# Kernel optimization log

Hardware: AMD Instinct MI355X
Metric: run time of the kernel (lower is better)

Reference implementation:

```python
import jax, jax.numpy as jnp
import numpy as np

NH, NKV, D = 16, 8, 128
HID = 2048
EPS = 1e-6
ROPE_BASE = 10000.0
T = 2048


def setup_inputs() -> dict:
    key = jax.random.key(0)
    k1, k2, k3 = jax.random.split(key, 3)
    return {
        "positions": jnp.arange(T, dtype=jnp.int32),
        "hidden_states": jax.random.normal(k1, (T, HID), dtype=jnp.float32),
        "w_qkv": jax.random.normal(k2, (HID, (NH + 2 * NKV) * D), dtype=jnp.float32) * 0.02,
        "w_o": jax.random.normal(k3, (NH * D, HID), dtype=jnp.float32) * 0.02,
        "q_norm_w": jnp.ones((D,), dtype=jnp.float32),
        "k_norm_w": jnp.ones((D,), dtype=jnp.float32),
    }


def _rmsnorm(x, w):
    # per-head RMSNorm over last dim (head_dim)
    return x * jax.lax.rsqrt(jnp.mean(x * x, axis=-1, keepdims=True) + EPS) * w


def reference(positions, hidden_states, w_qkv, w_o, q_norm_w, k_norm_w):
    t = hidden_states.shape[0]
    scale = D ** -0.5

    # fused QKV projection, then split
    qkv = hidden_states @ w_qkv                       # [T, (NH+2*NKV)*D]
    q, k, v = jnp.split(qkv, [NH * D, (NH + NKV) * D], axis=-1)
    q = q.reshape(t, NH, D)
    k = k.reshape(t, NKV, D)
    v = v.reshape(t, NKV, D)

    # per-head QK RMSNorm (Qwen3)
    q = _rmsnorm(q, q_norm_w)
    k = _rmsnorm(k, k_norm_w)

    # RoPE (neox style: rotate half-split pairs)
    inv_freq = 1.0 / (ROPE_BASE ** (jnp.arange(0, D, 2, dtype=jnp.float32) / D))
    freqs = positions.astype(jnp.float32)[:, None] * inv_freq  # [T, D/2]
    cos = jnp.cos(freqs)[:, None, :]                   # [T, 1, D/2]
    sin = jnp.sin(freqs)[:, None, :]

    def rope(x):
        x1, x2 = jnp.split(x, 2, axis=-1)
        return jnp.concatenate([x1 * cos - x2 * sin, x2 * cos + x1 * sin], axis=-1)

    q = rope(q)
    k = rope(k)

    # GQA: repeat kv heads
    g = NH // NKV
    kr = jnp.repeat(k, g, axis=1)                      # [T, NH, D]
    vr = jnp.repeat(v, g, axis=1)

    # causal attention
    scores = jnp.einsum('thd,shd->hts', q, kr) * scale  # [NH, T, T]
    causal = jnp.tril(jnp.ones((t, t), dtype=bool))
    scores = jnp.where(causal[None], scores, -jnp.inf)
    probs = jax.nn.softmax(scores, axis=-1)
    o = jnp.einsum('hts,shd->thd', probs, vr).reshape(t, NH * D)

    return o @ w_o
```

## Files before the change

kernel.cpp:

```cpp
#include <hip/hip_runtime.h>
#include <math.h>

#define T_TOK 2048
#define HIDDEN 2048
#define NH 16
#define NKV 8
#define DH 128

typedef unsigned short u16;
typedef __attribute__((ext_vector_type(8))) short bf16x8;
typedef __attribute__((ext_vector_type(4))) float f32x4;

__device__ __forceinline__ u16 f2bf(float f) {
  union { float f; unsigned u; } x; x.f = f;
  unsigned r = (x.u + 0x7fffu + ((x.u >> 16) & 1u)) >> 16;
  return (u16)r;
}

__device__ __forceinline__ void gload16(const void* g, void* l) {
  __builtin_amdgcn_global_load_lds((const __attribute__((address_space(1))) void*)g,
                                   (__attribute__((address_space(3))) void*)l,
                                   16, 0, 0);
}

__global__ __launch_bounds__(256) void prepass(const float* __restrict__ hidden,
                                               const float* __restrict__ w_qkv,
                                               const float* __restrict__ w_o,
                                               u16* __restrict__ Xb,
                                               u16* __restrict__ WqkvT,
                                               u16* __restrict__ WoT) {
  __shared__ float tile[64][65];
  const int b = blockIdx.x;
  if (b < 4096) {
    int i = b * 256 + threadIdx.x;
    float4 v = ((const float4*)hidden)[i];
    ushort4 o;
    o.x = f2bf(v.x); o.y = f2bf(v.y); o.z = f2bf(v.z); o.w = f2bf(v.w);
    ((ushort4*)Xb)[i] = o;
    return;
  }
  const float* in; u16* out; int R, Cdim, c0, r0;
  if (b < 6144) {
    int bb = b - 4096;
    in = w_qkv; out = WqkvT; R = 2048; Cdim = 4096;
    c0 = (bb & 63) * 64; r0 = (bb >> 6) * 64;
  } else {
    int bb = b - 6144;
    in = w_o; out = WoT; R = 2048; Cdim = 2048;
    c0 = (bb & 31) * 64; r0 = (bb >> 5) * 64;
  }
  const int tx = threadIdx.x & 63, ty = threadIdx.x >> 6;
#pragma unroll
  for (int i = 0; i < 64; i += 4)
    tile[ty + i][tx] = in[(size_t)(r0 + ty + i) * Cdim + c0 + tx];
  __syncthreads();
#pragma unroll
  for (int i = 0; i < 64; i += 4)
    out[(size_t)(c0 + ty + i) * R + r0 + tx] = f2bf(tile[tx][ty + i]);
}

__global__ __launch_bounds__(256) void add_f32_vec(const float* __restrict__ a,
                                                   const float* __restrict__ b,
                                                   float* __restrict__ o, int n4) {
  int i = blockIdx.x * blockDim.x + threadIdx.x;
  if (i < n4) {
    float4 x = ((const float4*)a)[i], y = ((const float4*)b)[i];
    float4 z = {x.x + y.x, x.y + y.y, x.z + y.z, x.w + y.w};
    ((float4*)o)[i] = z;
  }
}

__global__ __launch_bounds__(256) void rope_vt(const float* __restrict__ qkv,
                                               const int* __restrict__ pos,
                                               const float* __restrict__ qw,
                                               const float* __restrict__ kw,
                                               u16* __restrict__ Qg,
                                               u16* __restrict__ Kg,
                                               u16* __restrict__ Vt,
                                               unsigned* __restrict__ counter) {
  __shared__ float tile[64][65];
  const int b = blockIdx.x;
  if (b < 12288) {
    const int wave = threadIdx.x >> 6, j = threadIdx.x & 63;
    const int idx = b * 4 + wave;
    const int t = idx & 2047, slot = idx >> 11;
    const float QSC = 0.088388347648318447f * 1.4426950408889634f;
    const float* src = qkv + (size_t)t * 4096 + slot * 128;
    float x1 = src[j], x2 = src[j + 64];
    float ss = x1 * x1 + x2 * x2;
#pragma unroll
    for (int m = 1; m < 64; m <<= 1) ss += __shfl_xor(ss, m);
    float r = rsqrtf(ss * (1.0f / 128.0f) + 1e-6f);
    const bool isq = slot < NH;
    const float* w = isq ? qw : kw;
    float xn1 = x1 * r * w[j], xn2 = x2 * r * w[j + 64];
    float fp = (float)pos[t];
    float inv_freq = exp2f(-(float)j * (13.287712379549449f / 64.0f));
    float ang = fp * inv_freq;
    float sn, cs;
    sincosf(ang, &sn, &cs);
    float o1 = xn1 * cs - xn2 * sn;
    float o2 = xn2 * cs + xn1 * sn;
    if (isq) {
      size_t base = ((size_t)slot * T_TOK + t) * DH;
      Qg[base + j] = f2bf(o1 * QSC); Qg[base + 64 + j] = f2bf(o2 * QSC);
    } else {
      size_t base = ((size_t)(slot - NH) * T_TOK + t) * DH;
      Kg[base + j] = f2bf(o1); Kg[base + 64 + j] = f2bf(o2);
    }
    return;
  }
  if (b == 12288 && threadIdx.x == 0) *counter = 0u;
  const int bb = b - 12288;
  const int h = bb & 7, rest = bb >> 3;
  const int t0 = (rest & 31) * 64, d0 = (rest >> 5) * 64;
  const int tx = threadIdx.x & 63, ty = threadIdx.x >> 6;
#pragma unroll
  for (int i = 0; i < 64; i += 4)
    tile[ty + i][tx] = qkv[(size_t)(t0 + ty + i) * 4096 + (NH + NKV) * DH + h * DH + d0 + tx];
  __syncthreads();
#pragma unroll
  for (int i = 0; i < 64; i += 4)
    Vt[((size_t)h * DH + d0 + ty + i) * T_TOK + t0 + tx] = f2bf(tile[tx][ty + i]);
}

__global__ __launch_bounds__(256) void gemm_bf16(const u16* __restrict__ A,
                                                 const u16* __restrict__ Bt,
                                                 float* __restrict__ C,
                                                 int M, int N, int K, int lda, int ldb) {
  __shared__ u16 Alds[128 * 32];
  __shared__ u16 Blds[128 * 32];
  A += (size_t)blockIdx.z * K;
  Bt += (size_t)blockIdx.z * K;
  C += (size_t)blockIdx.z * M * N;
  const int m0 = blockIdx.y * 128, n0 = blockIdx.x * 128;
  const int wave = threadIdx.x >> 6, lane = threadIdx.x & 63;
  const int l15 = lane & 15, quad = lane >> 4;
  const int wr = wave >> 1, wc = wave & 1;

  const f32x4 zero = {0.f, 0.f, 0.f, 0.f};
  f32x4 acc[4][4];
#pragma unroll
  for (int i = 0; i < 4; ++i)
#pragma unroll
    for (int j = 0; j < 4; ++j) acc[i][j] = zero;

  for (int k0 = 0; k0 < K; k0 += 32) {
    __syncthreads();
#pragma unroll
    for (int c = 0; c < 2; ++c) {
      int chunk = wave * 2 + c;
      int slot = chunk * 64 + lane;
      int row = slot >> 2;
      int g = (slot & 3) ^ (row & 3);
      gload16(A + (size_t)(m0 + row) * lda + k0 + g * 8, &Alds[chunk * 512]);
      gload16(Bt + (size_t)(n0 + row) * ldb + k0 + g * 8, &Blds[chunk * 512]);
    }
    __syncthreads();
    bf16x8 af[4], bfr[4];
#pragma unroll
    for (int mt = 0; mt < 4; ++mt) {
      int r = wr * 64 + mt * 16 + l15;
      af[mt] = *(const bf16x8*)&Alds[r * 32 + ((quad ^ (r & 3)) * 8)];
    }
#pragma unroll
    for (int nt = 0; nt < 4; ++nt) {
      int r = wc * 64 + nt * 16 + l15;
      bfr[nt] = *(const bf16x8*)&Blds[r * 32 + ((quad ^ (r & 3)) * 8)];
    }
#pragma unroll
    for (int mt = 0; mt < 4; ++mt)
#pragma unroll
      for (int nt = 0; nt < 4; ++nt)
        acc[mt][nt] = __builtin_amdgcn_mfma_f32_16x16x32_bf16(af[mt], bfr[nt], acc[mt][nt], 0, 0, 0);
  }
#pragma unroll
  for (int mt = 0; mt < 4; ++mt)
#pragma unroll
    for (int nt = 0; nt < 4; ++nt)
#pragma unroll
      for (int r = 0; r < 4; ++r)
        C[(size_t)(m0 + wr * 64 + mt * 16 + quad * 4 + r) * N + n0 + wc * 64 + nt * 16 + l15] =
            acc[mt][nt][r];
}

__global__ __launch_bounds__(256) void attn_kernel(const u16* __restrict__ Qg,
                                                   const u16* __restrict__ Kg,
                                                   const u16* __restrict__ Vtg,
                                                   float* __restrict__ Opart,
                                                   float* __restrict__ Lpart,
                                                   unsigned* __restrict__ counter) {
  __shared__ u16 Klds[64 * 128];
  __shared__ u16 Vlds[128 * 64];
  __shared__ u16 Plds[4][16 * 72];
  __shared__ unsigned item_s;
  const int wave = threadIdx.x >> 6, lane = threadIdx.x & 63;
  const int l15 = lane & 15, quad = lane >> 4;
  u16* Pw = &Plds[wave][0];
  const f32x4 zero = {0.f, 0.f, 0.f, 0.f};
  const float4 zero4 = {0.f, 0.f, 0.f, 0.f};

  for (;;) {
    __syncthreads();
    if (threadIdx.x == 0) item_s = atomicAdd(counter, 1u);
    __syncthreads();
    const unsigned item = item_s;
    if (item >= 1024u) break;
    const int qt = 31 - (int)(item >> 5);
    const int s  = (int)(item >> 4) & 1;
    const int h  = (int)item & 15;
    const int kvh = h >> 1;
    const int slot = (h * 32 + qt) * 2 + s;
    const int j0 = s ? (qt + 2) >> 1 : 0;
    const int j1 = s ? qt + 1 : (qt + 2) >> 1;

    float* Oslot = Opart + (size_t)slot * (64 * 128);

    if (j0 >= j1) {
      for (int t = threadIdx.x; t < 64 * 128 / 4; t += 256) ((float4*)Oslot)[t] = zero4;
      if (threadIdx.x < 64) Lpart[slot * 64 + threadIdx.x] = 0.f;
      continue;
    }

    const u16* Qh = Qg + (size_t)h * T_TOK * DH;
    const u16* Kh = Kg + (size_t)kvh * T_TOK * DH;
    const u16* Vh = Vtg + (size_t)kvh * DH * T_TOK;
    const int qrow0 = qt * 64 + wave * 16;

    bf16x8 qf[4];
#pragma unroll
    for (int ks = 0; ks < 4; ++ks)
      qf[ks] = *(const bf16x8*)(Qh + (size_t)(qrow0 + l15) * DH + ks * 32 + quad * 8);

    f32x4 oacc[8];
#pragma unroll
    for (int i = 0; i < 8; ++i) oacc[i] = zero;
    float l_i[4] = {0.f, 0.f, 0.f, 0.f};

    for (int j = j0; j < j1; ++j) {
      __syncthreads();
#pragma unroll
      for (int c = 0; c < 4; ++c) {
        int chunk = wave * 4 + c;
        int sl = chunk * 64 + lane;
        {
          int ss = sl >> 4;
          int g = (sl & 15) ^ (ss & 15);
          gload16(Kh + ((size_t)(j * 64 + ss)) * DH + g * 8, &Klds[chunk * 512]);
        }
        {
          int d = sl >> 3;
          int g = (sl & 7) ^ (d & 7);
          gload16(Vh + (size_t)d * T_TOK + j * 64 + g * 8, &Vlds[chunk * 512]);
        }
      }
      __syncthreads();

      f32x4 sacc[4];
#pragma unroll
      for (int nt = 0; nt < 4; ++nt) sacc[nt] = zero;
#pragma unroll
      for (int nt = 0; nt < 4; ++nt) {
        int sr = nt * 16 + l15;
#pragma unroll
        for (int ks = 0; ks < 4; ++ks) {
          bf16x8 kf = *(const bf16x8*)&Klds[sr * 128 + (((ks * 4 + quad) ^ (sr & 15)) * 8)];
          sacc[nt] = __builtin_amdgcn_mfma_f32_16x16x32_bf16(qf[ks], kf, sacc[nt], 0, 0, 0);
        }
      }

      if (j == qt) {
#pragma unroll
        for (int nt = 0; nt < 4; ++nt)
#pragma unroll
          for (int r = 0; r < 4; ++r) {
            int col = j * 64 + nt * 16 + l15;
            int row = qrow0 + quad * 4 + r;
            if (col > row) sacc[nt][r] = -INFINITY;
          }
      }

#pragma unroll
      for (int nt = 0; nt < 4; ++nt)
#pragma unroll
        for (int r = 0; r < 4; ++r) {
          float pv = exp2f(sacc[nt][r]);
          unsigned u = __float_as_uint(pv);
          Pw[(quad * 4 + r) * 72 + nt * 16 + l15] = (u16)(u >> 16);
          l_i[r] += __uint_as_float(u & 0xffff0000u);
        }

      bf16x8 pf[2];
#pragma unroll
      for (int ks = 0; ks < 2; ++ks)
        pf[ks] = *(const bf16x8*)&Pw[l15 * 72 + ks * 32 + quad * 8];
#pragma unroll
      for (int ot = 0; ot < 8; ++ot) {
        int d = ot * 16 + l15;
#pragma unroll
        for (int ks = 0; ks < 2; ++ks) {
          bf16x8 vf = *(const bf16x8*)&Vlds[d * 64 + (((ks * 4 + quad) ^ (d & 7)) * 8)];
          oacc[ot] = __builtin_amdgcn_mfma_f32_16x16x32_bf16(pf[ks], vf, oacc[ot], 0, 0, 0);
        }
      }
    }

#pragma unroll
    for (int ot = 0; ot < 8; ++ot)
#pragma unroll
      for (int r = 0; r < 4; ++r)
        Oslot[(wave * 16 + quad * 4 + r) * 128 + ot * 16 + l15] = oacc[ot][r];
#pragma unroll
    for (int msk = 1; msk < 16; msk <<= 1)
#pragma unroll
      for (int r = 0; r < 4; ++r) l_i[r] += __shfl_xor(l_i[r], msk);
    if (l15 == 0) {
#pragma unroll
      for (int r = 0; r < 4; ++r)
        Lpart[slot * 64 + wave * 16 + quad * 4 + r] = l_i[r];
    }
  }
}

__global__ __launch_bounds__(256) void attn_merge(const float* __restrict__ Opart,
                                                  const float* __restrict__ Lpart,
                                                  u16* __restrict__ Og) {
  const int b = blockIdx.x;
  const int h = b & 15, qt = b >> 4;
  const int slot0 = (h * 32 + qt) * 2, slot1 = slot0 + 1;
  const float4* O0 = (const float4*)(Opart + (size_t)slot0 * (64 * 128));
  const float4* O1 = (const float4*)(Opart + (size_t)slot1 * (64 * 128));
#pragma unroll
  for (int it = 0; it < 8; ++it) {
    int idx = it * 256 + threadIdx.x;
    int r = idx >> 5, c4 = idx & 31;
    float rl = 1.0f / (Lpart[slot0 * 64 + r] + Lpart[slot1 * 64 + r]);
    float4 a = O0[idx], c = O1[idx];
    int row = qt * 64 + r, col = c4 * 4;
    u16* dst = Og + (size_t)row * (NH * DH) + h * DH + col;
    dst[0] = f2bf((a.x + c.x) * rl);
    dst[1] = f2bf((a.y + c.y) * rl);
    dst[2] = f2bf((a.z + c.z) * rl);
    dst[3] = f2bf((a.w + c.w) * rl);
  }
}

extern "C" void kernel_launch(void* const* d_in, const int* in_sizes, int n_in,
                              void* d_out, int out_size, void* d_ws, size_t ws_size,
                              hipStream_t stream) {
  (void)in_sizes; (void)n_in; (void)out_size; (void)ws_size;
  const int* positions = (const int*)d_in[0];
  const float* hidden  = (const float*)d_in[1];
  const float* w_qkv   = (const float*)d_in[2];
  const float* w_o     = (const float*)d_in[3];
  const float* q_norm  = (const float*)d_in[4];
  const float* k_norm  = (const float*)d_in[5];
  float* out = (float*)d_out;

  char* ws = (char*)d_ws;
  u16*   Xb    = (u16*)(ws);
  u16*   WqkvT = (u16*)(ws + ( 8ull << 20));
  u16*   WoT   = (u16*)(ws + (24ull << 20));
  float* QKV   = (float*)(ws + (32ull << 20));
  u16*   Qg    = (u16*)(ws + (64ull << 20));
  u16*   Kg    = (u16*)(ws + (72ull << 20));
  u16*   Vt    = (u16*)(ws + (76ull << 20));
  u16*   AttnO = (u16*)(ws + (80ull << 20));
  float* Opart = QKV;
  float* Lpart = (float*)(ws);
  unsigned* ctr = (unsigned*)(ws + (512ull << 10));
  float* G2P0  = QKV;
  float* G2P1  = QKV + 2048 * 2048;

  prepass<<<dim3(7168), 256, 0, stream>>>(hidden, w_qkv, w_o, Xb, WqkvT, WoT);

  gemm_bf16<<<dim3(4096 / 128, T_TOK / 128, 1), 256, 0, stream>>>(
      Xb, WqkvT, QKV, T_TOK, 4096, HIDDEN, HIDDEN, HIDDEN);

  rope_vt<<<dim3(12288 + 512), 256, 0, stream>>>(QKV, positions, q_norm, k_norm, Qg, Kg, Vt, ctr);

  attn_kernel<<<dim3(768), 256, 0, stream>>>(Qg, Kg, Vt, Opart, Lpart, ctr);
  attn_merge<<<dim3(512), 256, 0, stream>>>(Opart, Lpart, AttnO);

  gemm_bf16<<<dim3(HIDDEN / 128, T_TOK / 128, 2), 256, 0, stream>>>(
      AttnO, WoT, G2P0, T_TOK, HIDDEN, 1024, NH * DH, NH * DH);
  add_f32_vec<<<dim3(T_TOK * HIDDEN / 4 / 256), 256, 0, stream>>>(
      G2P0, G2P1, out, T_TOK * HIDDEN / 4);
}
```

Before: 272.2 us.

## Deepen GEMM K-tile to 64 and add split-K for QKV and output GEMMs

The bf16 GEMM now stages 64-wide K slices in LDS with an 8-way XOR swizzle and runs two MFMA sub-steps per barrier pair, which halves the number of synchronisations per K. When the workspace is large enough, the QKV projection is split along K into two partial outputs that rope_vt sums on load, and the output projection uses a 4-way split-K reduced by a generalized add kernel. These splits are meant to raise the number of blocks in flight, at the cost of extra fp32 partial traffic and larger LDS use per block.

```diff
diff --git a/kernel.cpp b/kernel.cpp
--- a/kernel.cpp
+++ b/kernel.cpp
@@ -59,18 +59,26 @@
     out[(size_t)(c0 + ty + i) * R + r0 + tx] = f2bf(tile[tx][ty + i]);
 }
 
-__global__ __launch_bounds__(256) void add_f32_vec(const float* __restrict__ a,
-                                                   const float* __restrict__ b,
-                                                   float* __restrict__ o, int n4) {
+__global__ __launch_bounds__(256) void add_parts(const float* __restrict__ a,
+                                                 const float* __restrict__ b,
+                                                 const float* __restrict__ c,
+                                                 const float* __restrict__ d,
+                                                 float* __restrict__ o, int n4, int nparts) {
   int i = blockIdx.x * blockDim.x + threadIdx.x;
   if (i < n4) {
     float4 x = ((const float4*)a)[i], y = ((const float4*)b)[i];
     float4 z = {x.x + y.x, x.y + y.y, x.z + y.z, x.w + y.w};
+    if (nparts == 4) {
+      float4 u = ((const float4*)c)[i], v = ((const float4*)d)[i];
+      z.x += u.x + v.x; z.y += u.y + v.y; z.z += u.z + v.z; z.w += u.w + v.w;
+    }
     ((float4*)o)[i] = z;
   }
 }
 
-__global__ __launch_bounds__(256) void rope_vt(const float* __restrict__ qkv,
+__global__ __launch_bounds__(256) void rope_vt(const float* __restrict__ qkv0,
+                                               const float* __restrict__ qkv1,
+                                               int sumP,
                                                const int* __restrict__ pos,
                                                const float* __restrict__ qw,
                                                const float* __restrict__ kw,
@@ -85,8 +93,9 @@
     const int idx = b * 4 + wave;
     const int t = idx & 2047, slot = idx >> 11;
     const float QSC = 0.088388347648318447f * 1.4426950408889634f;
-    const float* src = qkv + (size_t)t * 4096 + slot * 128;
-    float x1 = src[j], x2 = src[j + 64];
+    const size_t base_i = (size_t)t * 4096 + slot * 128;
+    float x1 = qkv0[base_i + j], x2 = qkv0[base_i + j + 64];
+    if (sumP) { x1 += qkv1[base_i + j]; x2 += qkv1[base_i + j + 64]; }
     float ss = x1 * x1 + x2 * x2;
 #pragma unroll
     for (int m = 1; m < 64; m <<= 1) ss += __shfl_xor(ss, m);
@@ -116,8 +125,12 @@
   const int t0 = (rest & 31) * 64, d0 = (rest >> 5) * 64;
   const int tx = threadIdx.x & 63, ty = threadIdx.x >> 6;
 #pragma unroll
-  for (int i = 0; i < 64; i += 4)
-    tile[ty + i][tx] = qkv[(size_t)(t0 + ty + i) * 4096 + (NH + NKV) * DH + h * DH + d0 + tx];
+  for (int i = 0; i < 64; i += 4) {
+    size_t gi = (size_t)(t0 + ty + i) * 4096 + (NH + NKV) * DH + h * DH + d0 + tx;
+    float v = qkv0[gi];
+    if (sumP) v += qkv1[gi];
+    tile[ty + i][tx] = v;
+  }
   __syncthreads();
 #pragma unroll
   for (int i = 0; i < 64; i += 4)
@@ -128,8 +141,8 @@
                                                  const u16* __restrict__ Bt,
                                                  float* __restrict__ C,
                                                  int M, int N, int K, int lda, int ldb) {
-  __shared__ u16 Alds[128 * 32];
-  __shared__ u16 Blds[128 * 32];
+  __shared__ u16 Alds[128 * 64];
+  __shared__ u16 Blds[128 * 64];
   A += (size_t)blockIdx.z * K;
   Bt += (size_t)blockIdx.z * K;
   C += (size_t)blockIdx.z * M * N;
@@ -145,34 +158,37 @@
 #pragma unroll
     for (int j = 0; j < 4; ++j) acc[i][j] = zero;
 
-  for (int k0 = 0; k0 < K; k0 += 32) {
+  for (int k0 = 0; k0 < K; k0 += 64) {
     __syncthreads();
 #pragma unroll
-    for (int c = 0; c < 2; ++c) {
-      int chunk = wave * 2 + c;
+    for (int c = 0; c < 4; ++c) {
+      int chunk = wave * 4 + c;
       int slot = chunk * 64 + lane;
-      int row = slot >> 2;
-      int g = (slot & 3) ^ (row & 3);
+      int row = slot >> 3;
+      int g = (slot & 7) ^ (row & 7);
       gload16(A + (size_t)(m0 + row) * lda + k0 + g * 8, &Alds[chunk * 512]);
       gload16(Bt + (size_t)(n0 + row) * ldb + k0 + g * 8, &Blds[chunk * 512]);
     }
     __syncthreads();
-    bf16x8 af[4], bfr[4];
-#pragma unroll
-    for (int mt = 0; mt < 4; ++mt) {
-      int r = wr * 64 + mt * 16 + l15;
-      af[mt] = *(const bf16x8*)&Alds[r * 32 + ((quad ^ (r & 3)) * 8)];
-    }
-#pragma unroll
-    for (int nt = 0; nt < 4; ++nt) {
-      int r = wc * 64 + nt * 16 + l15;
-      bfr[nt] = *(const bf16x8*)&Blds[r * 32 + ((quad ^ (r & 3)) * 8)];
-    }
-#pragma unroll
-    for (int mt = 0; mt < 4; ++mt)
-#pragma unroll
-      for (int nt = 0; nt < 4; ++nt)
-        acc[mt][nt] = __builtin_amdgcn_mfma_f32_16x16x32_bf16(af[mt], bfr[nt], acc[mt][nt], 0, 0, 0);
+#pragma unroll
+    for (int ksub = 0; ksub < 2; ++ksub) {
+      bf16x8 af[4], bfr[4];
+#pragma unroll
+      for (int mt = 0; mt < 4; ++mt) {
+        int r = wr * 64 + mt * 16 + l15;
+        af[mt] = *(const bf16x8*)&Alds[r * 64 + (((ksub * 4 + quad) ^ (r & 7)) * 8)];
+      }
+#pragma unroll
+      for (int nt = 0; nt < 4; ++nt) {
+        int r = wc * 64 + nt * 16 + l15;
+        bfr[nt] = *(const bf16x8*)&Blds[r * 64 + (((ksub * 4 + quad) ^ (r & 7)) * 8)];
+      }
+#pragma unroll
+      for (int mt = 0; mt < 4; ++mt)
+#pragma unroll
+        for (int nt = 0; nt < 4; ++nt)
+          acc[mt][nt] = __builtin_amdgcn_mfma_f32_16x16x32_bf16(af[mt], bfr[nt], acc[mt][nt], 0, 0, 0);
+    }
   }
 #pragma unroll
   for (int mt = 0; mt < 4; ++mt)
@@ -348,7 +364,7 @@
 extern "C" void kernel_launch(void* const* d_in, const int* in_sizes, int n_in,
                               void* d_out, int out_size, void* d_ws, size_t ws_size,
                               hipStream_t stream) {
-  (void)in_sizes; (void)n_in; (void)out_size; (void)ws_size;
+  (void)in_sizes; (void)n_in; (void)out_size;
   const int* positions = (const int*)d_in[0];
   const float* hidden  = (const float*)d_in[1];
   const float* w_qkv   = (const float*)d_in[2];
@@ -357,33 +373,46 @@
   const float* k_norm  = (const float*)d_in[5];
   float* out = (float*)d_out;
 
+  const bool big = ws_size >= (121ull << 20);
   char* ws = (char*)d_ws;
   u16*   Xb    = (u16*)(ws);
   u16*   WqkvT = (u16*)(ws + ( 8ull << 20));
   u16*   WoT   = (u16*)(ws + (24ull << 20));
-  float* QKV   = (float*)(ws + (32ull << 20));
-  u16*   Qg    = (u16*)(ws + (64ull << 20));
-  u16*   Kg    = (u16*)(ws + (72ull << 20));
-  u16*   Vt    = (u16*)(ws + (76ull << 20));
-  u16*   AttnO = (u16*)(ws + (80ull << 20));
-  float* Opart = QKV;
+  float* P0    = (float*)(ws + (32ull << 20));
+  float* P1    = big ? (float*)(ws + (64ull << 20)) : P0;
+  size_t tb    = big ? (96ull << 20) : (64ull << 20);
+  u16*   Qg    = (u16*)(ws + tb);
+  u16*   Kg    = (u16*)(ws + tb + (8ull << 20));
+  u16*   Vt    = (u16*)(ws + tb + (12ull << 20));
+  u16*   AttnO = (u16*)(ws + tb + (16ull << 20));
+  float* Opart = P0;
   float* Lpart = (float*)(ws);
   unsigned* ctr = (unsigned*)(ws + (512ull << 10));
-  float* G2P0  = QKV;
-  float* G2P1  = QKV + 2048 * 2048;
+  float* G2P   = P0;
 
   prepass<<<dim3(7168), 256, 0, stream>>>(hidden, w_qkv, w_o, Xb, WqkvT, WoT);
 
-  gemm_bf16<<<dim3(4096 / 128, T_TOK / 128, 1), 256, 0, stream>>>(
-      Xb, WqkvT, QKV, T_TOK, 4096, HIDDEN, HIDDEN, HIDDEN);
-
-  rope_vt<<<dim3(12288 + 512), 256, 0, stream>>>(QKV, positions, q_norm, k_norm, Qg, Kg, Vt, ctr);
+  if (big) {
+    gemm_bf16<<<dim3(4096 / 128, T_TOK / 128, 2), 256, 0, stream>>>(
+        Xb, WqkvT, P0, T_TOK, 4096, 1024, HIDDEN, HIDDEN);
+  } else {
+    gemm_bf16<<<dim3(4096 / 128, T_TOK / 128, 1), 256, 0, stream>>>(
+        Xb, WqkvT, P0, T_TOK, 4096, 2048, HIDDEN, HIDDEN);
+  }
+
+  rope_vt<<<dim3(12288 + 512), 256, 0, stream>>>(P0, P1, big ? 1 : 0, positions,
+                                                 q_norm, k_norm, Qg, Kg, Vt, ctr);
 
   attn_kernel<<<dim3(768), 256, 0, stream>>>(Qg, Kg, Vt, Opart, Lpart, ctr);
   attn_merge<<<dim3(512), 256, 0, stream>>>(Opart, Lpart, AttnO);
 
-  gemm_bf16<<<dim3(HIDDEN / 128, T_TOK / 128, 2), 256, 0, stream>>>(
-      AttnO, WoT, G2P0, T_TOK, HIDDEN, 1024, NH * DH, NH * DH);
-  add_f32_vec<<<dim3(T_TOK * HIDDEN / 4 / 256), 256, 0, stream>>>(
-      G2P0, G2P1, out, T_TOK * HIDDEN / 4);
-}
+  const int sk2 = big ? 4 : 2;
+  const int kk2 = 2048 / sk2;
+  gemm_bf16<<<dim3(HIDDEN / 128, T_TOK / 128, sk2), 256, 0, stream>>>(
+      AttnO, WoT, G2P, T_TOK, HIDDEN, kk2, NH * DH, NH * DH);
+  const int n4 = T_TOK * HIDDEN / 4;
+  const float* g2p1 = G2P + 1 * T_TOK * HIDDEN;
+  const float* g2p2 = G2P + (sk2 > 2 ? 2 : 0) * (size_t)T_TOK * HIDDEN;
+  const float* g2p3 = G2P + (sk2 > 2 ? 3 : 0) * (size_t)T_TOK * HIDDEN;
+  add_parts<<<dim3(n4 / 256), 256, 0, stream>>>(G2P, g2p1, g2p2, g2p3, out, n4, sk2);
+}
```

Result: no change. 269.9 us (-0.9%).
